# Optimization experiments

Measured on AMD Instinct MI355X. Metric: run time of the kernel, lower is better.

Reference implementation:

```python
import jax, jax.numpy as jnp
import numpy as np

VOCAB = 4000
U = 30000   # unique tokens
M = 12      # max mid-char length
H = 256     # hidden_size
O = 768     # output_size
B = 16      # sequences
L = 2048    # tokens per sequence (equal lengths -> jit-friendly reassemble)


def setup_inputs() -> dict:
    key = jax.random.key(0)
    ks = jax.random.split(key, 8)
    emb_table = jax.random.normal(ks[0], (VOCAB, H), dtype=jnp.float32)
    emb_table = emb_table.at[0].set(0.0)  # padding_idx=0
    head_w = jax.random.normal(ks[1], (3 * H, O), dtype=jnp.float32) * 0.02
    head_b = jax.random.normal(ks[2], (O,), dtype=jnp.float32) * 0.02
    first = jax.random.randint(ks[3], (U,), 0, VOCAB, dtype=jnp.int32)
    mid = jax.random.randint(ks[4], (U, M), 0, VOCAB, dtype=jnp.int32)
    last = jax.random.randint(ks[5], (U,), 0, VOCAB, dtype=jnp.int32)
    inv_i = jax.random.randint(ks[6], (B * L,), 0, U, dtype=jnp.int32)
    return {"emb_table": emb_table, "head_w": head_w, "head_b": head_b,
            "first": first, "mid": mid, "last": last, "inv_i": inv_i,
            "batch": B, "seq_len": L}


def reference(emb_table, head_w, head_b, first, mid, last, inv_i, batch, seq_len):
    def lookup(ids):
        # emulate padding_idx=0: id 0 contributes a zero vector
        v = emb_table[ids]
        return v * (ids != 0)[..., None].astype(v.dtype)

    rep = jnp.concatenate(
        [lookup(first), lookup(mid).sum(axis=1), lookup(last)], axis=-1)  # [U, 3H]
    out = rep @ head_w + head_b                                           # [U, O]
    tok = out[inv_i].reshape(batch, seq_len, -1)                          # [B, L, O]
    # reassemble: one zero row before and after each sequence (F.pad (1,1) on time)
    return jnp.pad(tok, ((0, 0), (1, 1), (0, 0)))                         # [B, L+2, O]
```

## Files before the change

### kernel.cpp

```cpp
#include <hip/hip_runtime.h>

#define VOCAB 4000
#define UNIQ 30000
#define MIDN 12
#define HID 256
#define OUT 768
#define BATCH 16
#define SEQ 2048

#define NXCD 8
#define XCOLS 96
#define SUBC 16
#define TCHUNK 2048
#define NCHUNK 16
#define TPASS 256
#define NPASS 8
#define PLANE 32008

typedef __attribute__((ext_vector_type(8))) short short8;
typedef __attribute__((ext_vector_type(2))) float f32x2;
typedef __attribute__((ext_vector_type(4))) float f32x4;
typedef __attribute__((ext_vector_type(4))) unsigned int u32x4;
typedef __attribute__((ext_vector_type(4))) unsigned short u16x4;

__device__ __forceinline__ float bitsf(unsigned int x) {
    float f; __builtin_memcpy(&f, &x, 4); return f;
}
__device__ __forceinline__ unsigned short f2bf(float f) {
    unsigned int x;
    __builtin_memcpy(&x, &f, 4);
    x += 0x7fff + ((x >> 16) & 1);
    return (unsigned short)(x >> 16);
}

__global__ __launch_bounds__(256) void prep(
    const float* __restrict__ W, unsigned short* __restrict__ Wt,
    const int* __restrict__ first, const int* __restrict__ mid,
    const int* __restrict__ last, const int* __restrict__ inv_i,
    short* __restrict__ idsT,
    const float* __restrict__ E, unsigned short* __restrict__ Ebf)
{
    __shared__ float T[32][33];
    if (blockIdx.z < 3) {
        const int s  = blockIdx.z;
        const int n0 = blockIdx.x * 32;
        const int h0 = blockIdx.y * 32;
        const int tx = threadIdx.x & 31;
        const int ty = threadIdx.x >> 5;
        #pragma unroll
        for (int k = 0; k < 4; ++k) {
            int h = ty + 8 * k;
            T[h][tx] = W[(size_t)(s * HID + h0 + h) * OUT + n0 + tx];
        }
        __syncthreads();
        #pragma unroll
        for (int k = 0; k < 4; ++k) {
            int n = ty + 8 * k;
            Wt[(size_t)(s * OUT + n0 + n) * HID + h0 + tx] = f2bf(T[tx][n]);
        }
    } else if (blockIdx.z == 3) {
        int bid2 = blockIdx.y * 24 + blockIdx.x;
        int t = bid2 * 256 + threadIdx.x;
        if (t >= BATCH * SEQ) return;
        int u = inv_i[t];
        int4 m0 = *reinterpret_cast<const int4*>(&mid[u * MIDN]);
        int4 m1 = *reinterpret_cast<const int4*>(&mid[u * MIDN + 4]);
        int4 m2 = *reinterpret_cast<const int4*>(&mid[u * MIDN + 8]);
        short ids[16];
        ids[0]  = (short)first[u];
        ids[1]  = (short)m0.x; ids[2]  = (short)m0.y; ids[3]  = (short)m0.z; ids[4]  = (short)m0.w;
        ids[5]  = (short)m1.x; ids[6]  = (short)m1.y; ids[7]  = (short)m1.z; ids[8]  = (short)m1.w;
        ids[9]  = (short)m2.x; ids[10] = (short)m2.y; ids[11] = (short)m2.z; ids[12] = (short)m2.w;
        ids[13] = (short)last[u];
        ids[14] = 0; ids[15] = 0;
        *reinterpret_cast<short8*>(&idsT[(size_t)t * 16])     = *reinterpret_cast<short8*>(&ids[0]);
        *reinterpret_cast<short8*>(&idsT[(size_t)t * 16 + 8]) = *reinterpret_cast<short8*>(&ids[8]);
    } else {
        int bid2 = (blockIdx.z - 4) * 192 + blockIdx.y * 24 + blockIdx.x;
        int i = bid2 * 256 + threadIdx.x;
        if (i >= VOCAB * HID / 8) return;
        f32x4 e0 = *reinterpret_cast<const f32x4*>(&E[(size_t)i * 8]);
        f32x4 e1 = *reinterpret_cast<const f32x4*>(&E[(size_t)i * 8 + 4]);
        short8 v;
        v[0] = (short)f2bf(e0.x); v[1] = (short)f2bf(e0.y);
        v[2] = (short)f2bf(e0.z); v[3] = (short)f2bf(e0.w);
        v[4] = (short)f2bf(e1.x); v[5] = (short)f2bf(e1.y);
        v[6] = (short)f2bf(e1.z); v[7] = (short)f2bf(e1.w);
        *reinterpret_cast<short8*>(&Ebf[(size_t)i * 8]) = v;
    }
}

__global__ __launch_bounds__(256) void proj_mfma(
    const unsigned short* __restrict__ Ebf,
    const unsigned short* __restrict__ Wt,
    unsigned short* __restrict__ P,
    unsigned short* __restrict__ Pmid)
{
    const int s     = blockIdx.z;
    const int vbase = blockIdx.x * 128;
    const int cbase = blockIdx.y * 128;
    const unsigned short* Wts = Wt + (size_t)s * OUT * HID;

    __shared__ short As[128][40];
    __shared__ short Bs[128][40];

    const int tid  = threadIdx.x;
    const int lane = tid & 63;
    const int w    = tid >> 6;
    const int wm   = w >> 1;
    const int wn   = w & 1;
    const int lo   = lane & 15;
    const int hi   = lane >> 4;

    f32x4 acc[4][4] = {};

    for (int kt = 0; kt < HID; kt += 32) {
        #pragma unroll
        for (int p = 0; p < 2; ++p) {
            int idx = p * 256 + tid;
            int row = idx >> 2;
            int ko  = (idx & 3) * 8;
            short8 v = *reinterpret_cast<const short8*>(
                &Wts[(size_t)(cbase + row) * HID + kt + ko]);
            *reinterpret_cast<short8*>(&As[row][ko]) = v;
        }
        #pragma unroll
        for (int p = 0; p < 2; ++p) {
            int idx = p * 256 + tid;
            int row = idx >> 2;
            int ko  = (idx & 3) * 8;
            int gv  = vbase + row;
            short8 v = {};
            if (gv < VOCAB)
                v = *reinterpret_cast<const short8*>(&Ebf[(size_t)gv * HID + kt + ko]);
            *reinterpret_cast<short8*>(&Bs[row][ko]) = v;
        }
        __syncthreads();

        short8 a[4], b[4];
        #pragma unroll
        for (int f = 0; f < 4; ++f)
            a[f] = *reinterpret_cast<short8*>(&As[wm * 64 + f * 16 + lo][hi * 8]);
        #pragma unroll
        for (int f = 0; f < 4; ++f)
            b[f] = *reinterpret_cast<short8*>(&Bs[wn * 64 + f * 16 + lo][hi * 8]);
        #pragma unroll
        for (int fm = 0; fm < 4; ++fm)
            #pragma unroll
            for (int fn = 0; fn < 4; ++fn)
                acc[fm][fn] = __builtin_amdgcn_mfma_f32_16x16x32_bf16(
                    a[fm], b[fn], acc[fm][fn], 0, 0, 0);
        __syncthreads();
    }

    #pragma unroll
    for (int fm = 0; fm < 4; ++fm) {
        #pragma unroll
        for (int fn = 0; fn < 4; ++fn) {
            const int c0 = cbase + wm * 64 + fm * 16 + hi * 4;
            const int v  = vbase + wn * 64 + fn * 16 + lo;
            if (v < VOCAB) {
                u16x4 vals;
                vals.x = f2bf(acc[fm][fn][0]);
                vals.y = f2bf(acc[fm][fn][1]);
                vals.z = f2bf(acc[fm][fn][2]);
                vals.w = f2bf(acc[fm][fn][3]);
                if (s == 1) {
                    *reinterpret_cast<u16x4*>(
                        &Pmid[((size_t)(c0 >> 4) * VOCAB + v) * SUBC + (c0 & 15)]) = vals;
                } else {
                    const int so = (s == 0) ? 0 : 1;
                    const unsigned int sl = (unsigned int)c0 / XCOLS;
                    const unsigned int cc = (unsigned int)c0 - sl * XCOLS;
                    *reinterpret_cast<u16x4*>(
                        &P[(((size_t)sl * 2 + so) * VOCAB + v) * XCOLS + cc]) = vals;
                }
            }
        }
    }
}

extern __shared__ char lds_raw[];

__global__ __launch_bounds__(1024) void token_lds(
    const unsigned short* __restrict__ P,
    const unsigned short* __restrict__ Pmid,
    const short* __restrict__ idsT,
    const float* __restrict__ bias,
    float* __restrict__ out)
{
    const int xcd = blockIdx.x & 7;
    const int bi  = blockIdx.x >> 3;

    const int tid = threadIdx.x;
    const int l4  = tid & 3;
    const int grp = tid >> 2;

    char* myplane = lds_raw + l4 * PLANE;
    const unsigned short* Pbase = P + (size_t)xcd * 2 * VOCAB * XCOLS;

    if (bi == 0 && tid < 768) {
        int r  = tid / 24;
        int c4 = tid % 24;
        int b  = r >> 1;
        int row = (r & 1) ? (b * (SEQ + 2) + SEQ + 1) : (b * (SEQ + 2));
        f32x4 z = {};
        *reinterpret_cast<f32x4*>(
            &out[(size_t)row * OUT + xcd * XCOLS + c4 * 4]) = z;
    }

    int cur_sl = -1;

    #pragma unroll 1
    for (int k = 0; k < 3; ++k) {
        const int task = bi * 3 + k;
        const int sl   = task >> 4;
        const int ch   = task & 15;

        if (sl != cur_sl) {
            if (cur_sl >= 0) __syncthreads();
            const int sub = xcd * 6 + sl;
            const unsigned short* src = Pmid + (size_t)sub * VOCAB * SUBC;
            #pragma unroll
            for (int i = 0; i < 16; ++i) {
                int idx = i * 1024 + tid;
                if (idx < VOCAB * 4) {
                    int row = idx >> 2;
                    int q   = idx & 3;
                    uint2 v = *reinterpret_cast<const uint2*>(&src[row * SUBC + q * 4]);
                    *reinterpret_cast<uint2*>(lds_raw + q * PLANE + row * 8) = v;
                }
            }
            __syncthreads();
            cur_sl = sl;
        }

        const int csub = sl * SUBC + l4 * 4;
        const int colc = xcd * XCOLS + csub;
        const unsigned short* P0 = Pbase + csub;
        const unsigned short* P2 = Pbase + (size_t)VOCAB * XCOLS + csub;
        const f32x4 bv = *reinterpret_cast<const f32x4*>(&bias[colc]);

        const int t0 = ch * TCHUNK + grp;
        float* dstT = out + ((size_t)(ch * (SEQ + 2) + 1 + grp)) * OUT + colc;

#define LDIDS(lo_, hi_, tt_) { \
        const u32x4* _r = reinterpret_cast<const u32x4*>(&idsT[(size_t)(tt_) * 16]); \
        lo_ = _r[0]; hi_ = _r[1]; }

#define GATHER(fv_, lv_, lo_, hi_) { \
        int _fid = (int)((lo_).x & 0xffffu); \
        int _lid = (int)((hi_).z >> 16); \
        fv_ = *reinterpret_cast<const uint2*>(&P0[(size_t)_fid * XCOLS]); \
        lv_ = *reinterpret_cast<const uint2*>(&P2[(size_t)_lid * XCOLS]); }

        u32x4 ilA, ihA, ilB, ihB;
        uint2 fvA, lvA, fvB, lvB;

        LDIDS(ilA, ihA, t0);
        LDIDS(ilB, ihB, t0 + TPASS);
        GATHER(fvA, lvA, ilA, ihA);

        #pragma unroll
        for (int p = 0; p < NPASS; ++p) {
            const bool even = (p & 1) == 0;
            u32x4 clo = even ? ilA : ilB;
            u32x4 chi = even ? ihA : ihB;
            uint2 cfv = even ? fvA : fvB;
            uint2 clv = even ? lvA : lvB;

            if (p + 1 < NPASS) {
                if (even) { GATHER(fvB, lvB, ilB, ihB); }
                else      { GATHER(fvA, lvA, ilA, ihA); }
            }
            if (p + 2 < NPASS) {
                if (even) { LDIDS(ilA, ihA, t0 + (p + 2) * TPASS); }
                else      { LDIDS(ilB, ihB, t0 + (p + 2) * TPASS); }
            }

            int rid[MIDN];
            rid[0]  = (int)(clo.x >> 16);
            rid[1]  = (int)(clo.y & 0xffffu);
            rid[2]  = (int)(clo.y >> 16);
            rid[3]  = (int)(clo.z & 0xffffu);
            rid[4]  = (int)(clo.z >> 16);
            rid[5]  = (int)(clo.w & 0xffffu);
            rid[6]  = (int)(clo.w >> 16);
            rid[7]  = (int)(chi.x & 0xffffu);
            rid[8]  = (int)(chi.x >> 16);
            rid[9]  = (int)(chi.y & 0xffffu);
            rid[10] = (int)(chi.y >> 16);
            rid[11] = (int)(chi.z & 0xffffu);

            uint2 mv[MIDN];
            #pragma unroll
            for (int m = 0; m < MIDN; ++m)
                mv[m] = *reinterpret_cast<const uint2*>(myplane + rid[m] * 8);

            f32x2 acc01 = {bv.x, bv.y};
            f32x2 acc23 = {bv.z, bv.w};
            #pragma unroll
            for (int m = 0; m < MIDN; ++m) {
                f32x2 v0 = {bitsf(mv[m].x << 16), bitsf(mv[m].x & 0xffff0000u)};
                f32x2 v1 = {bitsf(mv[m].y << 16), bitsf(mv[m].y & 0xffff0000u)};
                acc01 += v0;
                acc23 += v1;
            }
            {
                f32x2 v0 = {bitsf(cfv.x << 16), bitsf(cfv.x & 0xffff0000u)};
                f32x2 v1 = {bitsf(cfv.y << 16), bitsf(cfv.y & 0xffff0000u)};
                acc01 += v0; acc23 += v1;
                f32x2 w0 = {bitsf(clv.x << 16), bitsf(clv.x & 0xffff0000u)};
                f32x2 w1 = {bitsf(clv.y << 16), bitsf(clv.y & 0xffff0000u)};
                acc01 += w0; acc23 += w1;
            }

            float* dst = dstT + (size_t)p * (TPASS * OUT);
            f32x4 o = {acc01.x, acc01.y, acc23.x, acc23.y};
            __builtin_nontemporal_store(o, reinterpret_cast<f32x4*>(dst));
        }
#undef LDIDS
#undef GATHER
    }
}

extern "C" void kernel_launch(void* const* d_in, const int* in_sizes, int n_in,
                              void* d_out, int out_size, void* d_ws, size_t ws_size,
                              hipStream_t stream)
{
    const float* emb    = (const float*)d_in[0];
    const float* head_w = (const float*)d_in[1];
    const float* head_b = (const float*)d_in[2];
    const int*   first  = (const int*)d_in[3];
    const int*   mid    = (const int*)d_in[4];
    const int*   last   = (const int*)d_in[5];
    const int*   inv_i  = (const int*)d_in[6];
    float* out = (float*)d_out;

    char* ws = (char*)d_ws;
    unsigned short* P    = (unsigned short*)ws;
    unsigned short* Wt   = (unsigned short*)(ws + 12288000);
    unsigned short* Ebf  = (unsigned short*)(ws + 13467648);
    unsigned short* Pmid = (unsigned short*)(ws + 15515648);
    short*          idsT = (short*)(ws + 21659648);

    dim3 gp(24, 8, 7);
    prep<<<gp, 256, 0, stream>>>(head_w, Wt, first, mid, last, inv_i,
                                 idsT, emb, Ebf);

    dim3 g1(32, 6, 3);
    proj_mfma<<<g1, 256, 0, stream>>>(Ebf, Wt, P, Pmid);

    token_lds<<<256, 1024, 4 * PLANE, stream>>>(P, Pmid, idsT, head_b, out);
}
```

Baseline: 60.13 us.

## Halve per-block column slice to shrink LDS and double the block count

The token gather kernel now gives each block 8-column slices of the mid-projection table instead of 16. That halves the LDS plane size and launches twice as many blocks, aiming for more resident blocks per CU and more parallelism. The hand-written double-buffered prefetch of ids and first/last gathers is replaced by a simple non-unrolled loop, and the staging loop is no longer unrolled. In exchange, every token's 32-byte id record is read twice as often overall, and each output store is narrower (8 bytes per thread), which gives shorter contiguous write segments. Removing the manual prefetch also loses memory latency overlap.

```diff
diff --git a/kernel.cpp b/kernel.cpp
--- a/kernel.cpp
+++ b/kernel.cpp
@@ -11,11 +11,12 @@
 #define NXCD 8
 #define XCOLS 96
 #define SUBC 16
+#define SUB8 8
 #define TCHUNK 2048
 #define NCHUNK 16
 #define TPASS 256
 #define NPASS 8
-#define PLANE 32008
+#define PLANE8 16004
 
 typedef __attribute__((ext_vector_type(8))) short short8;
 typedef __attribute__((ext_vector_type(2))) float f32x2;
@@ -182,7 +183,7 @@
 
 extern __shared__ char lds_raw[];
 
-__global__ __launch_bounds__(1024) void token_lds(
+__global__ __launch_bounds__(1024, 8) void token_lds8(
     const unsigned short* __restrict__ P,
     const unsigned short* __restrict__ Pmid,
     const short* __restrict__ idsT,
@@ -196,7 +197,7 @@
     const int l4  = tid & 3;
     const int grp = tid >> 2;
 
-    char* myplane = lds_raw + l4 * PLANE;
+    char* myplane = lds_raw + l4 * PLANE8;
     const unsigned short* Pbase = P + (size_t)xcd * 2 * VOCAB * XCOLS;
 
     if (bi == 0 && tid < 768) {
@@ -219,108 +220,73 @@
 
         if (sl != cur_sl) {
             if (cur_sl >= 0) __syncthreads();
-            const int sub = xcd * 6 + sl;
-            const unsigned short* src = Pmid + (size_t)sub * VOCAB * SUBC;
-            #pragma unroll
+            const int sub16 = (xcd * 12 + sl) >> 1;
+            const int half  = (xcd * 12 + sl) & 1;
+            const unsigned short* src =
+                Pmid + ((size_t)sub16 * VOCAB) * SUBC + half * 8;
+            #pragma unroll 1
             for (int i = 0; i < 16; ++i) {
                 int idx = i * 1024 + tid;
                 if (idx < VOCAB * 4) {
                     int row = idx >> 2;
                     int q   = idx & 3;
-                    uint2 v = *reinterpret_cast<const uint2*>(&src[row * SUBC + q * 4]);
-                    *reinterpret_cast<uint2*>(lds_raw + q * PLANE + row * 8) = v;
+                    unsigned int v = *reinterpret_cast<const unsigned int*>(
+                        &src[(size_t)row * SUBC + q * 2]);
+                    *reinterpret_cast<unsigned int*>(
+                        lds_raw + q * PLANE8 + row * 4) = v;
                 }
             }
             __syncthreads();
             cur_sl = sl;
         }
 
-        const int csub = sl * SUBC + l4 * 4;
+        const int csub = sl * SUB8 + l4 * 2;
         const int colc = xcd * XCOLS + csub;
         const unsigned short* P0 = Pbase + csub;
         const unsigned short* P2 = Pbase + (size_t)VOCAB * XCOLS + csub;
-        const f32x4 bv = *reinterpret_cast<const f32x4*>(&bias[colc]);
+        const f32x2 bv = *reinterpret_cast<const f32x2*>(&bias[colc]);
 
         const int t0 = ch * TCHUNK + grp;
         float* dstT = out + ((size_t)(ch * (SEQ + 2) + 1 + grp)) * OUT + colc;
 
-#define LDIDS(lo_, hi_, tt_) { \
-        const u32x4* _r = reinterpret_cast<const u32x4*>(&idsT[(size_t)(tt_) * 16]); \
-        lo_ = _r[0]; hi_ = _r[1]; }
-
-#define GATHER(fv_, lv_, lo_, hi_) { \
-        int _fid = (int)((lo_).x & 0xffffu); \
-        int _lid = (int)((hi_).z >> 16); \
-        fv_ = *reinterpret_cast<const uint2*>(&P0[(size_t)_fid * XCOLS]); \
-        lv_ = *reinterpret_cast<const uint2*>(&P2[(size_t)_lid * XCOLS]); }
-
-        u32x4 ilA, ihA, ilB, ihB;
-        uint2 fvA, lvA, fvB, lvB;
-
-        LDIDS(ilA, ihA, t0);
-        LDIDS(ilB, ihB, t0 + TPASS);
-        GATHER(fvA, lvA, ilA, ihA);
-
-        #pragma unroll
+        #pragma unroll 1
         for (int p = 0; p < NPASS; ++p) {
-            const bool even = (p & 1) == 0;
-            u32x4 clo = even ? ilA : ilB;
-            u32x4 chi = even ? ihA : ihB;
-            uint2 cfv = even ? fvA : fvB;
-            uint2 clv = even ? lvA : lvB;
-
-            if (p + 1 < NPASS) {
-                if (even) { GATHER(fvB, lvB, ilB, ihB); }
-                else      { GATHER(fvA, lvA, ilA, ihA); }
-            }
-            if (p + 2 < NPASS) {
-                if (even) { LDIDS(ilA, ihA, t0 + (p + 2) * TPASS); }
-                else      { LDIDS(ilB, ihB, t0 + (p + 2) * TPASS); }
-            }
-
-            int rid[MIDN];
-            rid[0]  = (int)(clo.x >> 16);
-            rid[1]  = (int)(clo.y & 0xffffu);
-            rid[2]  = (int)(clo.y >> 16);
-            rid[3]  = (int)(clo.z & 0xffffu);
-            rid[4]  = (int)(clo.z >> 16);
-            rid[5]  = (int)(clo.w & 0xffffu);
-            rid[6]  = (int)(clo.w >> 16);
-            rid[7]  = (int)(chi.x & 0xffffu);
-            rid[8]  = (int)(chi.x >> 16);
-            rid[9]  = (int)(chi.y & 0xffffu);
-            rid[10] = (int)(chi.y >> 16);
-            rid[11] = (int)(chi.z & 0xffffu);
-
-            uint2 mv[MIDN];
-            #pragma unroll
-            for (int m = 0; m < MIDN; ++m)
-                mv[m] = *reinterpret_cast<const uint2*>(myplane + rid[m] * 8);
-
-            f32x2 acc01 = {bv.x, bv.y};
-            f32x2 acc23 = {bv.z, bv.w};
-            #pragma unroll
-            for (int m = 0; m < MIDN; ++m) {
-                f32x2 v0 = {bitsf(mv[m].x << 16), bitsf(mv[m].x & 0xffff0000u)};
-                f32x2 v1 = {bitsf(mv[m].y << 16), bitsf(mv[m].y & 0xffff0000u)};
-                acc01 += v0;
-                acc23 += v1;
-            }
-            {
-                f32x2 v0 = {bitsf(cfv.x << 16), bitsf(cfv.x & 0xffff0000u)};
-                f32x2 v1 = {bitsf(cfv.y << 16), bitsf(cfv.y & 0xffff0000u)};
-                acc01 += v0; acc23 += v1;
-                f32x2 w0 = {bitsf(clv.x << 16), bitsf(clv.x & 0xffff0000u)};
-                f32x2 w1 = {bitsf(clv.y << 16), bitsf(clv.y & 0xffff0000u)};
-                acc01 += w0; acc23 += w1;
-            }
+            const int t = t0 + p * TPASS;
+            const u32x4* idr = reinterpret_cast<const u32x4*>(&idsT[(size_t)t * 16]);
+            u32x4 lo = idr[0];
+            u32x4 hi = idr[1];
+
+            int fid = (int)(lo.x & 0xffffu);
+            int lid = (int)(hi.z >> 16);
+            unsigned int fv = *reinterpret_cast<const unsigned int*>(
+                &P0[(size_t)fid * XCOLS]);
+            unsigned int lv = *reinterpret_cast<const unsigned int*>(
+                &P2[(size_t)lid * XCOLS]);
+
+            unsigned int mv0  = *reinterpret_cast<const unsigned int*>(myplane + (int)(lo.x >> 16)      * 4);
+            unsigned int mv1  = *reinterpret_cast<const unsigned int*>(myplane + (int)(lo.y & 0xffffu)  * 4);
+            unsigned int mv2  = *reinterpret_cast<const unsigned int*>(myplane + (int)(lo.y >> 16)      * 4);
+            unsigned int mv3  = *reinterpret_cast<const unsigned int*>(myplane + (int)(lo.z & 0xffffu)  * 4);
+            unsigned int mv4  = *reinterpret_cast<const unsigned int*>(myplane + (int)(lo.z >> 16)      * 4);
+            unsigned int mv5  = *reinterpret_cast<const unsigned int*>(myplane + (int)(lo.w & 0xffffu)  * 4);
+            unsigned int mv6  = *reinterpret_cast<const unsigned int*>(myplane + (int)(lo.w >> 16)      * 4);
+            unsigned int mv7  = *reinterpret_cast<const unsigned int*>(myplane + (int)(hi.x & 0xffffu)  * 4);
+            unsigned int mv8  = *reinterpret_cast<const unsigned int*>(myplane + (int)(hi.x >> 16)      * 4);
+            unsigned int mv9  = *reinterpret_cast<const unsigned int*>(myplane + (int)(hi.y & 0xffffu)  * 4);
+            unsigned int mv10 = *reinterpret_cast<const unsigned int*>(myplane + (int)(hi.y >> 16)      * 4);
+            unsigned int mv11 = *reinterpret_cast<const unsigned int*>(myplane + (int)(hi.z & 0xffffu)  * 4);
+
+            f32x2 acc = {bv.x, bv.y};
+#define ADDW(w_) { f32x2 v_ = {bitsf((w_) << 16), bitsf((w_) & 0xffff0000u)}; acc += v_; }
+            ADDW(mv0)  ADDW(mv1)  ADDW(mv2)  ADDW(mv3)
+            ADDW(mv4)  ADDW(mv5)  ADDW(mv6)  ADDW(mv7)
+            ADDW(mv8)  ADDW(mv9)  ADDW(mv10) ADDW(mv11)
+            ADDW(fv)   ADDW(lv)
+#undef ADDW
 
             float* dst = dstT + (size_t)p * (TPASS * OUT);
-            f32x4 o = {acc01.x, acc01.y, acc23.x, acc23.y};
-            __builtin_nontemporal_store(o, reinterpret_cast<f32x4*>(dst));
-        }
-#undef LDIDS
-#undef GATHER
+            __builtin_nontemporal_store(acc, reinterpret_cast<f32x2*>(dst));
+        }
     }
 }
 
@@ -351,5 +317,5 @@
     dim3 g1(32, 6, 3);
     proj_mfma<<<g1, 256, 0, stream>>>(Ebf, Wt, P, Pmid);
 
-    token_lds<<<256, 1024, 4 * PLANE, stream>>>(P, Pmid, idsT, head_b, out);
-}
+    token_lds8<<<512, 1024, 4 * PLANE8, stream>>>(P, Pmid, idsT, head_b, out);
+}
```

New measurement: 179.4 us. +198.4%, slower.
